# Kernel optimization log

Measured on AMD Instinct MI355X. Metric: run time of the kernel, lower is better.

The kernel has to match this reference:

```python
import jax, jax.numpy as jnp
import numpy as np

N_DELAYS = 512
N_SAMPLES = 2 ** 15  # 32768


def _interp_linear(x, out_size):
    # F.interpolate(mode='linear', align_corners=False) on [B, C, L]
    L = x.shape[-1]
    scale = L / out_size
    pos = (jnp.arange(out_size, dtype=jnp.float32) + 0.5) * scale - 0.5
    pos = jnp.clip(pos, 0.0, L - 1)
    i0 = jnp.floor(pos).astype(jnp.int32)
    i1 = jnp.minimum(i0 + 1, L - 1)
    w = (pos - i0).astype(x.dtype)
    return x[..., i0] * (1.0 - w) + x[..., i1] * w


def _interp_nearest(x, out_size):
    # F.interpolate(mode='nearest') on [B, C, L]: idx = floor(j * L/out)
    L = x.shape[-1]
    idx = jnp.clip(jnp.floor(jnp.arange(out_size) * (L / out_size)).astype(jnp.int32), 0, L - 1)
    return x[..., idx]


def setup_inputs() -> dict:
    key = jax.random.key(0)
    k1, k2, k3, k4, k5 = jax.random.split(key, 5)
    batch = 8
    impulse = jax.random.normal(k1, (batch, 128), dtype=jnp.float32)
    delay_selection = jax.random.normal(k2, (batch, N_DELAYS, 16), dtype=jnp.float32)
    damping = jax.random.normal(k3, (batch, 1), dtype=jnp.float32)
    filt = jax.random.normal(k4, (batch, 16), dtype=jnp.float32)
    # torch forward draws uniform(-1,1) noise; passed as input for determinism
    noise = jax.random.uniform(k5, (batch, 1, N_SAMPLES), dtype=jnp.float32, minval=-1.0, maxval=1.0)
    # comb-filter buffer: delays[i, ::i+1] = 1
    delays_np = np.zeros((N_DELAYS, N_SAMPLES), dtype=np.float32)
    for i in range(N_DELAYS):
        delays_np[i, ::i + 1] = 1.0
    delays = jnp.asarray(delays_np)
    return {"impulse": impulse, "delay_selection": delay_selection, "damping": damping,
            "filt": filt, "noise": noise, "delays": delays}


def reference(impulse, delay_selection, damping, filt, noise, delays):
    batch = delay_selection.shape[0]
    n_delays, n_samples = delays.shape
    n_frames = filt.shape[-1]

    # filter spectrum envelope: sigmoid -> linear upsample to n_samples//2 -> pad 1
    f = jax.nn.sigmoid(filt).reshape(-1, 1, n_frames)
    f = _interp_linear(f, n_samples // 2)
    filt_spec = jnp.pad(f, ((0, 0), (0, 0), (0, 1)))  # [B,1,n_samples//2+1]

    # impulse: squared envelope upsampled, modulating uniform noise
    imp = impulse.reshape(batch, 1, -1) ** 2
    imp = _interp_linear(imp, n_samples) * noise  # [B,1,n_samples]

    # damping: powers = linspace(1, 1, n_frames) == ones (faithful to source)
    damp = jax.nn.sigmoid(damping.reshape(batch, 1)) * 0.9999
    powers = jnp.linspace(1.0, float(damp.shape[-1]), n_frames)
    damp = damp[:, :, None] ** powers[None, None, :]  # [B,1,n_frames]
    damp = _interp_nearest(damp, n_samples)  # [B,1,n_samples]

    # sparse comb selection: softmax over delays, nearest upsample, weighted sum
    ds = jax.nn.softmax(delay_selection.reshape(batch, n_delays, -1), axis=1)
    ds = _interp_nearest(ds, n_samples)  # [B,n_delays,n_samples]
    d = jnp.einsum('bdn,dn->bn', ds, delays)[:, None, :] * damp  # [B,1,n_samples]

    # FFT convolution
    delay_spec = jnp.fft.rfft(d, axis=-1, norm='ortho')
    impulse_spec = jnp.fft.rfft(imp, axis=-1, norm='ortho')
    spec = delay_spec * impulse_spec * filt_spec
    final = jnp.fft.irfft(spec, n=n_samples, axis=-1, norm='ortho')
    return final
```

## Files before the change

kernel.cpp:

```cpp
#include <hip/hip_runtime.h>
#include <math.h>

#define NSAMP 32768
#define NDEL  512
#define NFR   16
#define BATCH 8
#define TWO_PI 6.283185307179586f

__device__ __forceinline__ float2 cmul(float2 a, float2 b) {
    return make_float2(a.x*b.x - a.y*b.y, a.x*b.y + a.y*b.x);
}
__device__ __forceinline__ float2 cadd(float2 a, float2 b){ return make_float2(a.x+b.x, a.y+b.y); }
__device__ __forceinline__ float2 csub(float2 a, float2 b){ return make_float2(a.x-b.x, a.y-b.y); }
__device__ __forceinline__ float2 crot(float2 z, float sign){ return make_float2(-sign*z.y, sign*z.x); }

__device__ __forceinline__ int phi(int i){ return i + (i >> 3); }

__device__ __forceinline__ void bfly8(const float2 v[8], float sign, float2 X[8]) {
    const float S2 = 0.70710678118654752f;
    float2 t0 = cadd(v[0], v[4]), t1 = csub(v[0], v[4]);
    float2 t2 = cadd(v[2], v[6]), t3 = crot(csub(v[2], v[6]), sign);
    float2 E0 = cadd(t0, t2), E1 = cadd(t1, t3), E2 = csub(t0, t2), E3 = csub(t1, t3);
    float2 u0 = cadd(v[1], v[5]), u1 = csub(v[1], v[5]);
    float2 u2 = cadd(v[3], v[7]), u3 = crot(csub(v[3], v[7]), sign);
    float2 O0 = cadd(u0, u2), O1 = cadd(u1, u3), O2 = csub(u0, u2), O3 = csub(u1, u3);
    float2 c1 = make_float2( S2, sign*S2);
    float2 c3 = make_float2(-S2, sign*S2);
    float2 w1o = cmul(c1, O1);
    float2 w2o = crot(O2, sign);
    float2 w3o = cmul(c3, O3);
    X[0]=cadd(E0,O0);  X[4]=csub(E0,O0);
    X[1]=cadd(E1,w1o); X[5]=csub(E1,w1o);
    X[2]=cadd(E2,w2o); X[6]=csub(E2,w2o);
    X[3]=cadd(E3,w3o); X[7]=csub(E3,w3o);
}

__device__ __forceinline__ void twiddle_q(float2 v[8], float ang1) {
    float sa, ca; __sincosf(ang1, &sa, &ca);
    float2 w1 = make_float2(ca, sa), wq = w1;
#pragma unroll
    for (int q = 1; q < 8; ++q) { v[q] = cmul(v[q], wq); wq = cmul(wq, w1); }
}

__global__ void build_kernel(const float* __restrict__ impulse,
                             const float* __restrict__ dsel,
                             const float* __restrict__ damping,
                             const float* __restrict__ noise,
                             float2* __restrict__ A) {
    const int b = blockIdx.x >> 4, f = blockIdx.x & 15;
    const int tid = threadIdx.x;
    __shared__ float Wrow[NDEL];
    __shared__ float dl[2048];
    __shared__ float red[256];

    float v0 = dsel[(b*NDEL + tid)*NFR + f];
    float v1 = dsel[(b*NDEL + tid + 256)*NFR + f];
    red[tid] = fmaxf(v0, v1);
    __syncthreads();
    for (int off = 128; off > 0; off >>= 1) {
        if (tid < off) red[tid] = fmaxf(red[tid], red[tid+off]);
        __syncthreads();
    }
    float M = red[0];
    __syncthreads();
    float e0 = expf(v0 - M), e1 = expf(v1 - M);
    Wrow[tid] = e0; Wrow[tid+256] = e1;
    red[tid] = e0 + e1;
    __syncthreads();
    for (int off = 128; off > 0; off >>= 1) {
        if (tid < off) red[tid] += red[tid+off];
        __syncthreads();
    }
    float S = red[0];
    float damp = 1.0f/(1.0f + expf(-damping[b])) * 0.9999f;
    float scale = damp / S;
    Wrow[tid] *= scale; Wrow[tid+256] *= scale;
    for (int k = tid; k < 2048; k += 256) dl[k] = 0.0f;
    __syncthreads();

    const unsigned start = (unsigned)f << 11;
    const float fstart = (float)start;

    for (unsigned t = 1; t < 64; ++t) {
        float wt = Wrow[t-1];
        unsigned q0 = (unsigned)(__fdividef(fstart, (float)t));
        unsigned n0 = q0 * t;
        while (n0 < start) n0 += t;
        while (n0 >= start + t) n0 -= t;
        for (unsigned i = (n0 - start) + (unsigned)tid * t; i < 2048u; i += 256u * t)
            atomicAdd(&dl[i], wt);
    }
    for (unsigned t = 64u + (unsigned)tid; t <= 512u; t += 256u) {
        float wt = Wrow[t-1];
        unsigned q0 = (unsigned)(__fdividef(fstart, (float)t));
        unsigned n0 = q0 * t;
        while (n0 < start) n0 += t;
        while (n0 >= start + t) n0 -= t;
        for (unsigned i = n0 - start; i < 2048u; i += t)
            atomicAdd(&dl[i], wt);
    }
    __syncthreads();

    for (int k = tid; k < 2048; k += 256) {
        int n = (int)start + k;
        float pos = (n + 0.5f) * (1.0f/256.0f) - 0.5f;
        pos = fminf(fmaxf(pos, 0.0f), 127.0f);
        int i0 = (int)pos;
        float w = pos - (float)i0;
        int i1 = (i0 + 1 > 127) ? 127 : i0 + 1;
        float x0 = impulse[b*128 + i0]; x0 *= x0;
        float x1 = impulse[b*128 + i1]; x1 *= x1;
        float iv = (x0*(1.0f - w) + x1*w) * noise[b*NSAMP + n];
        A[b*NSAMP + n] = make_float2(dl[k], iv);
    }
}

__global__ void fft512_kernel(const float2* __restrict__ src,
                              float2* __restrict__ dst,
                              const float* __restrict__ filt,
                              float sign) {
    const int wave = threadIdx.x >> 6, j = threadIdx.x & 63;
    const int s = blockIdx.x >> 4;
    const int n2 = ((blockIdx.x & 15) << 2) | wave;
    __shared__ float2 buf[4][2][576];
    __shared__ float fs[NFR];
    if (filt && threadIdx.x < NFR)
        fs[threadIdx.x] = 1.0f/(1.0f + expf(-filt[s*NFR + threadIdx.x]));
    __syncthreads();

    const float2* sp = src + s * NSAMP;
    float2 v[8], X[8];
    if (!filt) {
#pragma unroll
        for (int q = 0; q < 8; ++q) v[q] = sp[64*j + 4096*q + n2];
    } else {
        const float SCALE = 1.0f / (32768.0f * 181.01933598375618f);
#pragma unroll
        for (int q = 0; q < 8; ++q) {
            int m = 64*j + 4096*q + n2;
            float2 Zk = sp[m];
            float2 Zr = sp[(NSAMP - m) & (NSAMP - 1)];
            float2 Zrc = make_float2(Zr.x, -Zr.y);
            float2 D = make_float2(0.5f*(Zk.x + Zrc.x), 0.5f*(Zk.y + Zrc.y));
            float2 df = make_float2(Zk.x - Zrc.x, Zk.y - Zrc.y);
            float2 I = make_float2(0.5f*df.y, -0.5f*df.x);
            int jjb = (m <= NSAMP - m) ? m : NSAMP - m;
            float fv = 0.0f;
            if (jjb < NSAMP/2) {
                float pos = (jjb + 0.5f) * (1.0f/1024.0f) - 0.5f;
                pos = fminf(fmaxf(pos, 0.0f), 15.0f);
                int i0 = (int)pos;
                float w = pos - (float)i0;
                int i1 = (i0 + 1 > 15) ? 15 : i0 + 1;
                fv = fs[i0]*(1.0f - w) + fs[i1]*w;
            }
            float2 spc = cmul(D, I);
            float g = fv * SCALE;
            v[q] = make_float2(spc.x * g, spc.y * g);
        }
    }

    bfly8(v, sign, X);
#pragma unroll
    for (int r = 0; r < 8; ++r) buf[wave][0][phi(8*j + r)] = X[r];
    __syncthreads();
#pragma unroll
    for (int q = 0; q < 8; ++q) v[q] = buf[wave][0][phi(j + 64*q)];
    int jm = j & 7;
    twiddle_q(v, sign * TWO_PI * (float)jm * (1.0f/64.0f));
    bfly8(v, sign, X);
#pragma unroll
    for (int r = 0; r < 8; ++r) buf[wave][1][phi(((j>>3)<<6) + jm + (r<<3))] = X[r];
    __syncthreads();
#pragma unroll
    for (int q = 0; q < 8; ++q) v[q] = buf[wave][1][phi(j + 64*q)];
    twiddle_q(v, sign * TWO_PI * (float)j * (1.0f/512.0f));
    bfly8(v, sign, X);

    float2* dp = dst + s * NSAMP + n2 * 512;
#pragma unroll
    for (int r = 0; r < 8; ++r) {
        int k1 = j + 64*r;
        int pr = (n2 * k1) & (NSAMP - 1);
        float sa, ca; __sincosf(sign * TWO_PI * (float)pr * (1.0f/32768.0f), &sa, &ca);
        dp[k1] = cmul(X[r], make_float2(ca, sa));
    }
}

__global__ void fft64_kernel(const float2* __restrict__ src,
                             float2* __restrict__ dst,
                             float* __restrict__ out_real,
                             float sign) {
    const int wave = threadIdx.x >> 6, l = threadIdx.x & 63;
    const int c = l & 7, jj = l >> 3;
    const int s = blockIdx.x >> 4;
    const int k1base = (((blockIdx.x & 15) << 2) | wave) << 3;
    __shared__ float2 buf[4][576];

    const float2* sp = src + s * NSAMP;
    float2 v[8], X[8];
#pragma unroll
    for (int q = 0; q < 8; ++q) v[q] = sp[(jj + 8*q)*512 + k1base + c];

    bfly8(v, sign, X);
#pragma unroll
    for (int r = 0; r < 8; ++r) buf[wave][phi(c*64 + jj*8 + r)] = X[r];
    __syncthreads();
#pragma unroll
    for (int q = 0; q < 8; ++q) v[q] = buf[wave][phi(c*64 + jj + 8*q)];
    twiddle_q(v, sign * TWO_PI * (float)jj * (1.0f/64.0f));
    bfly8(v, sign, X);

    int base = s * NSAMP + k1base + c;
    if (out_real) {
#pragma unroll
        for (int r = 0; r < 8; ++r) out_real[base + 512*(jj + 8*r)] = X[r].x;
    } else {
#pragma unroll
        for (int r = 0; r < 8; ++r) dst[base + 512*(jj + 8*r)] = X[r];
    }
}

extern "C" void kernel_launch(void* const* d_in, const int* in_sizes, int n_in,
                              void* d_out, int out_size, void* d_ws, size_t ws_size,
                              hipStream_t stream) {
    const float* impulse = (const float*)d_in[0];
    const float* dsel    = (const float*)d_in[1];
    const float* damping = (const float*)d_in[2];
    const float* filt    = (const float*)d_in[3];
    const float* noise   = (const float*)d_in[4];
    float* out = (float*)d_out;

    float2* A = (float2*)d_ws;
    float2* B = A + BATCH * NSAMP;

    build_kernel<<<dim3(BATCH*NFR), dim3(256), 0, stream>>>(impulse, dsel, damping, noise, A);
    fft512_kernel<<<dim3(128), dim3(256), 0, stream>>>(A, B, nullptr, -1.0f);
    fft64_kernel <<<dim3(128), dim3(256), 0, stream>>>(B, A, nullptr, -1.0f);
    fft512_kernel<<<dim3(128), dim3(256), 0, stream>>>(A, B, filt, 1.0f);
    fft64_kernel <<<dim3(128), dim3(256), 0, stream>>>(B, nullptr, out, 1.0f);
}
```

Before: 148.3 us.

## Split work into single-wave blocks to spread kernels across more CUs

Every kernel now launches 512 blocks of 64 threads instead of 128 blocks of 256. The FFT kernels become one wave per block with private shared buffers. The build kernel splits each 2048-sample frame into four 512-sample sub-blocks, each with its own softmax and comb scatter. The aim is to fill the many CUs on the device, where only 128 blocks were launched before, at the cost of repeating the softmax and delay-start computation four times per frame.

```diff
diff --git a/kernel.cpp b/kernel.cpp
--- a/kernel.cpp
+++ b/kernel.cpp
@@ -47,38 +47,46 @@
                              const float* __restrict__ damping,
                              const float* __restrict__ noise,
                              float2* __restrict__ A) {
-    const int b = blockIdx.x >> 4, f = blockIdx.x & 15;
+    const int b   = blockIdx.x >> 6;
+    const int f   = (blockIdx.x >> 2) & 15;
+    const int sub = blockIdx.x & 3;
     const int tid = threadIdx.x;
     __shared__ float Wrow[NDEL];
-    __shared__ float dl[2048];
-    __shared__ float red[256];
-
-    float v0 = dsel[(b*NDEL + tid)*NFR + f];
-    float v1 = dsel[(b*NDEL + tid + 256)*NFR + f];
-    red[tid] = fmaxf(v0, v1);
-    __syncthreads();
-    for (int off = 128; off > 0; off >>= 1) {
+    __shared__ float dl[512];
+    __shared__ float red[64];
+
+    float v[8], m = -1e30f;
+#pragma unroll
+    for (int k = 0; k < 8; ++k) {
+        v[k] = dsel[(b*NDEL + tid + 64*k)*NFR + f];
+        m = fmaxf(m, v[k]);
+    }
+    red[tid] = m;
+    __syncthreads();
+    for (int off = 32; off > 0; off >>= 1) {
         if (tid < off) red[tid] = fmaxf(red[tid], red[tid+off]);
         __syncthreads();
     }
     float M = red[0];
     __syncthreads();
-    float e0 = expf(v0 - M), e1 = expf(v1 - M);
-    Wrow[tid] = e0; Wrow[tid+256] = e1;
-    red[tid] = e0 + e1;
-    __syncthreads();
-    for (int off = 128; off > 0; off >>= 1) {
+    float e[8], s = 0.0f;
+#pragma unroll
+    for (int k = 0; k < 8; ++k) { e[k] = expf(v[k] - M); s += e[k]; }
+    red[tid] = s;
+    __syncthreads();
+    for (int off = 32; off > 0; off >>= 1) {
         if (tid < off) red[tid] += red[tid+off];
         __syncthreads();
     }
     float S = red[0];
     float damp = 1.0f/(1.0f + expf(-damping[b])) * 0.9999f;
     float scale = damp / S;
-    Wrow[tid] *= scale; Wrow[tid+256] *= scale;
-    for (int k = tid; k < 2048; k += 256) dl[k] = 0.0f;
-    __syncthreads();
-
-    const unsigned start = (unsigned)f << 11;
+#pragma unroll
+    for (int k = 0; k < 8; ++k) Wrow[tid + 64*k] = e[k] * scale;
+    for (int k = tid; k < 512; k += 64) dl[k] = 0.0f;
+    __syncthreads();
+
+    const unsigned start = ((unsigned)f << 11) + ((unsigned)sub << 9);
     const float fstart = (float)start;
 
     for (unsigned t = 1; t < 64; ++t) {
@@ -87,21 +95,21 @@
         unsigned n0 = q0 * t;
         while (n0 < start) n0 += t;
         while (n0 >= start + t) n0 -= t;
-        for (unsigned i = (n0 - start) + (unsigned)tid * t; i < 2048u; i += 256u * t)
+        for (unsigned i = (n0 - start) + (unsigned)tid * t; i < 512u; i += 64u * t)
             atomicAdd(&dl[i], wt);
     }
-    for (unsigned t = 64u + (unsigned)tid; t <= 512u; t += 256u) {
+    for (unsigned t = 64u + (unsigned)tid; t <= 512u; t += 64u) {
         float wt = Wrow[t-1];
         unsigned q0 = (unsigned)(__fdividef(fstart, (float)t));
         unsigned n0 = q0 * t;
         while (n0 < start) n0 += t;
         while (n0 >= start + t) n0 -= t;
-        for (unsigned i = n0 - start; i < 2048u; i += t)
+        for (unsigned i = n0 - start; i < 512u; i += t)
             atomicAdd(&dl[i], wt);
     }
     __syncthreads();
 
-    for (int k = tid; k < 2048; k += 256) {
+    for (int k = tid; k < 512; k += 64) {
         int n = (int)start + k;
         float pos = (n + 0.5f) * (1.0f/256.0f) - 0.5f;
         pos = fminf(fmaxf(pos, 0.0f), 127.0f);
@@ -119,13 +127,13 @@
                               float2* __restrict__ dst,
                               const float* __restrict__ filt,
                               float sign) {
-    const int wave = threadIdx.x >> 6, j = threadIdx.x & 63;
-    const int s = blockIdx.x >> 4;
-    const int n2 = ((blockIdx.x & 15) << 2) | wave;
-    __shared__ float2 buf[4][2][576];
+    const int j  = threadIdx.x;
+    const int s  = blockIdx.x >> 6;
+    const int n2 = blockIdx.x & 63;
+    __shared__ float2 buf[2][576];
     __shared__ float fs[NFR];
-    if (filt && threadIdx.x < NFR)
-        fs[threadIdx.x] = 1.0f/(1.0f + expf(-filt[s*NFR + threadIdx.x]));
+    if (filt && j < NFR)
+        fs[j] = 1.0f/(1.0f + expf(-filt[s*NFR + j]));
     __syncthreads();
 
     const float2* sp = src + s * NSAMP;
@@ -162,18 +170,18 @@
 
     bfly8(v, sign, X);
 #pragma unroll
-    for (int r = 0; r < 8; ++r) buf[wave][0][phi(8*j + r)] = X[r];
-    __syncthreads();
-#pragma unroll
-    for (int q = 0; q < 8; ++q) v[q] = buf[wave][0][phi(j + 64*q)];
+    for (int r = 0; r < 8; ++r) buf[0][phi(8*j + r)] = X[r];
+    __syncthreads();
+#pragma unroll
+    for (int q = 0; q < 8; ++q) v[q] = buf[0][phi(j + 64*q)];
     int jm = j & 7;
     twiddle_q(v, sign * TWO_PI * (float)jm * (1.0f/64.0f));
     bfly8(v, sign, X);
 #pragma unroll
-    for (int r = 0; r < 8; ++r) buf[wave][1][phi(((j>>3)<<6) + jm + (r<<3))] = X[r];
-    __syncthreads();
-#pragma unroll
-    for (int q = 0; q < 8; ++q) v[q] = buf[wave][1][phi(j + 64*q)];
+    for (int r = 0; r < 8; ++r) buf[1][phi(((j>>3)<<6) + jm + (r<<3))] = X[r];
+    __syncthreads();
+#pragma unroll
+    for (int q = 0; q < 8; ++q) v[q] = buf[1][phi(j + 64*q)];
     twiddle_q(v, sign * TWO_PI * (float)j * (1.0f/512.0f));
     bfly8(v, sign, X);
 
@@ -191,11 +199,11 @@
                              float2* __restrict__ dst,
                              float* __restrict__ out_real,
                              float sign) {
-    const int wave = threadIdx.x >> 6, l = threadIdx.x & 63;
+    const int l = threadIdx.x;
     const int c = l & 7, jj = l >> 3;
-    const int s = blockIdx.x >> 4;
-    const int k1base = (((blockIdx.x & 15) << 2) | wave) << 3;
-    __shared__ float2 buf[4][576];
+    const int s = blockIdx.x >> 6;
+    const int k1base = (blockIdx.x & 63) << 3;
+    __shared__ float2 buf[576];
 
     const float2* sp = src + s * NSAMP;
     float2 v[8], X[8];
@@ -204,10 +212,10 @@
 
     bfly8(v, sign, X);
 #pragma unroll
-    for (int r = 0; r < 8; ++r) buf[wave][phi(c*64 + jj*8 + r)] = X[r];
-    __syncthreads();
-#pragma unroll
-    for (int q = 0; q < 8; ++q) v[q] = buf[wave][phi(c*64 + jj + 8*q)];
+    for (int r = 0; r < 8; ++r) buf[phi(c*64 + jj*8 + r)] = X[r];
+    __syncthreads();
+#pragma unroll
+    for (int q = 0; q < 8; ++q) v[q] = buf[phi(c*64 + jj + 8*q)];
     twiddle_q(v, sign * TWO_PI * (float)jj * (1.0f/64.0f));
     bfly8(v, sign, X);
 
@@ -234,9 +242,9 @@
     float2* A = (float2*)d_ws;
     float2* B = A + BATCH * NSAMP;
 
-    build_kernel<<<dim3(BATCH*NFR), dim3(256), 0, stream>>>(impulse, dsel, damping, noise, A);
-    fft512_kernel<<<dim3(128), dim3(256), 0, stream>>>(A, B, nullptr, -1.0f);
-    fft64_kernel <<<dim3(128), dim3(256), 0, stream>>>(B, A, nullptr, -1.0f);
-    fft512_kernel<<<dim3(128), dim3(256), 0, stream>>>(A, B, filt, 1.0f);
-    fft64_kernel <<<dim3(128), dim3(256), 0, stream>>>(B, nullptr, out, 1.0f);
-}
+    build_kernel<<<dim3(512), dim3(64), 0, stream>>>(impulse, dsel, damping, noise, A);
+    fft512_kernel<<<dim3(512), dim3(64), 0, stream>>>(A, B, nullptr, -1.0f);
+    fft64_kernel <<<dim3(512), dim3(64), 0, stream>>>(B, A, nullptr, -1.0f);
+    fft512_kernel<<<dim3(512), dim3(64), 0, stream>>>(A, B, filt, 1.0f);
+    fft64_kernel <<<dim3(512), dim3(64), 0, stream>>>(B, nullptr, out, 1.0f);
+}
```

Result: faster. 143.2 us (-3.4%).
